# Optimization experiments

Measured on AMD Instinct MI355X. Metric: run time of the kernel, lower is better.

The kernel has to match this reference:

```python
import jax, jax.numpy as jnp
import numpy as np

D_MODEL = 1024
N_HEAD = 16


def setup_inputs() -> dict:
    key = jax.random.key(0)
    ks = jax.random.split(key, 13)
    B, S, D = 2, 2048, D_MODEL
    scale = 1.0 / np.sqrt(D)
    inp = {
        "q": jax.random.normal(ks[0], (B, S, D), jnp.float32),
        "k": jax.random.normal(ks[1], (B, S, D), jnp.float32),
        "v": jax.random.normal(ks[2], (B, S, D), jnp.float32),
        "mask": jax.random.randint(ks[3], (1, 1, S, S), 0, 2, jnp.int32),
        "Wq": jax.random.normal(ks[4], (D, D), jnp.float32) * scale,
        "bq": jnp.zeros((D,), jnp.float32),
        "Wk": jax.random.normal(ks[5], (D, D), jnp.float32) * scale,
        "bk": jnp.zeros((D,), jnp.float32),
        "Wv": jax.random.normal(ks[6], (D, D), jnp.float32) * scale,
        "bv": jnp.zeros((D,), jnp.float32),
        "Wo": jax.random.normal(ks[7], (D, D), jnp.float32) * scale,
        "bo": jnp.zeros((D,), jnp.float32),
    }
    return inp


def _split_heads(x, n_head):
    # [B, S, D] -> [B, H, S, Dh]
    B, S, D = x.shape
    return x.reshape(B, S, n_head, D // n_head).transpose(0, 2, 1, 3)


def reference(q, k, v, mask, Wq, bq, Wk, bk, Wv, bv, Wo, bo):
    # linear projections (torch Linear: x @ W.T + b)
    qp = q @ Wq.T + bq
    kp = k @ Wk.T + bk
    vp = v @ Wv.T + bv
    qh = _split_heads(qp, N_HEAD)  # [B,H,S,Dh]
    kh = _split_heads(kp, N_HEAD)
    vh = _split_heads(vp, N_HEAD)
    d_k = qh.shape[-1]
    scores = jnp.einsum("bhqd,bhkd->bhqk", qh, kh) / jnp.sqrt(jnp.asarray(d_k, qh.dtype))
    neg = jnp.finfo(qh.dtype).min
    scores = jnp.where(mask == 0, neg, scores)
    attn = jax.nn.softmax(scores, axis=-1)
    out = jnp.einsum("bhqk,bhkd->bhqd", attn, vh)  # [B,H,S,Dh]
    B, H, S, Dh = out.shape
    concat = out.transpose(0, 2, 1, 3).reshape(B, S, H * Dh)
    return concat @ Wo.T + bo
```

## Files before the change

### kernel.cpp

```cpp
#include <hip/hip_runtime.h>
#include <hip/hip_bf16.h>

typedef __attribute__((ext_vector_type(8))) short short8;
typedef __attribute__((ext_vector_type(4))) float f32x4;
typedef __attribute__((ext_vector_type(4))) float floatv4;
typedef __attribute__((ext_vector_type(4))) unsigned int u32x4;
typedef unsigned short u16;
typedef unsigned int u32;
typedef unsigned long long u64;

#define S_LEN 2048
#define DMODEL 1024
#define NHEAD 16
#define DHEAD 64

__device__ __forceinline__ u16 f2bf(float f) {
  __hip_bfloat16 h = __float2bfloat16(f);
  return __builtin_bit_cast(u16, h);
}

__device__ __forceinline__ u32 cvtpk(float lo, float hi) {
  u32 r;
  asm("v_cvt_pk_bf16_f32 %0, %1, %2" : "=v"(r) : "v"(lo), "v"(hi));
  return r;
}

__device__ __forceinline__ void gload16(const void* g, void* l) {
  __builtin_amdgcn_global_load_lds(
      (const __attribute__((address_space(1))) u32*)g,
      (__attribute__((address_space(3))) u32*)l, 16, 0, 0);
}

__device__ __forceinline__ f32x4 mfma16(short8 a, short8 b, f32x4 c) {
  return __builtin_amdgcn_mfma_f32_16x16x32_bf16(a, b, c, 0, 0, 0);
}

__global__ void k_convert_qkv(const float* __restrict__ q, const float* __restrict__ k,
                              const float* __restrict__ v, u16* __restrict__ qb,
                              u16* __restrict__ kb, u16* __restrict__ vb) {
  const float* src = blockIdx.y == 0 ? q : blockIdx.y == 1 ? k : v;
  u16* dst = blockIdx.y == 0 ? qb : blockIdx.y == 1 ? kb : vb;
  int i = blockIdx.x * blockDim.x + threadIdx.x;
  floatv4 w = reinterpret_cast<const floatv4*>(src)[i];
  ushort4 o;
  o.x = f2bf(w.x); o.y = f2bf(w.y); o.z = f2bf(w.z); o.w = f2bf(w.w);
  reinterpret_cast<ushort4*>(dst)[i] = o;
}

__global__ void k_convert_w(const float* __restrict__ w0, const float* __restrict__ w1,
                            const float* __restrict__ w2, const float* __restrict__ w3,
                            u16* __restrict__ d0, u16* __restrict__ d1,
                            u16* __restrict__ d2, u16* __restrict__ d3) {
  const int z = blockIdx.y;
  const float* src = z == 0 ? w0 : z == 1 ? w1 : z == 2 ? w2 : w3;
  u16* dst = z == 0 ? d0 : z == 1 ? d1 : z == 2 ? d2 : d3;
  int i = blockIdx.x * blockDim.x + threadIdx.x;
  floatv4 w = reinterpret_cast<const floatv4*>(src)[i];
  ushort4 o;
  o.x = f2bf(w.x); o.y = f2bf(w.y); o.z = f2bf(w.z); o.w = f2bf(w.w);
  reinterpret_cast<ushort4*>(dst)[i] = o;
}

__global__ void k_maskpack(const int* __restrict__ mask, u64* __restrict__ bits) {
  int tid = blockIdx.x * blockDim.x + threadIdx.x;
  u64 b = __ballot(mask[tid] != 0);
  if ((threadIdx.x & 63) == 0) bits[tid >> 6] = b;
}

template <int BN>
__device__ __forceinline__ void gemm_body(const u16* __restrict__ A,
                                          const u16* __restrict__ W,
                                          const float* __restrict__ bias,
                                          void* __restrict__ dst, int mode,
                                          float scale) {
  constexpr int BM = 128, BK = 32, K = DMODEL;
  constexpr int MI = (BN == 128) ? 4 : 2;
  __shared__ u16 As[2][BM * BK];
  __shared__ u16 Bs[2][BN * BK];
  const int t = threadIdx.x;
  const int lane = t & 63, w = t >> 6;
  const int lr = lane & 15, lg = lane >> 4;
  const int wrow = (BN == 128) ? (w >> 1) * 64 : w * 32;
  const int wcol = (BN == 128) ? (w & 1) * 64 : 0;
  const int brow = blockIdx.y * BM, bcol = blockIdx.x * BN;

  const int sr = t >> 2, scg = (t & 3) * 8;
  const u16* Abase = A + (size_t)(brow + sr) * K + scg;
  const u16* Wbase = W + (size_t)(bcol + sr) * K + scg;

  f32x4 acc[MI][4] = {};

  auto stage = [&](int buf, int kt) {
    const int k0 = kt * BK;
    gload16(Abase + k0, &As[buf][w * 512]);
    gload16(Abase + (size_t)64 * K + k0, &As[buf][2048 + w * 512]);
    gload16(Wbase + k0, &Bs[buf][w * 512]);
    if constexpr (BN == 128)
      gload16(Wbase + (size_t)64 * K + k0, &Bs[buf][2048 + w * 512]);
  };

  stage(0, 0);
  __syncthreads();

  int cur = 0;
  constexpr int NT = K / BK;
  for (int kt = 0; kt < NT; ++kt) {
    if (kt + 1 < NT) stage(cur ^ 1, kt + 1);
    short8 af[MI], bfr[4];
#pragma unroll
    for (int i = 0; i < MI; ++i)
      af[i] = *(const short8*)&As[cur][(wrow + i * 16 + lr) * BK + lg * 8];
#pragma unroll
    for (int j = 0; j < 4; ++j)
      bfr[j] = *(const short8*)&Bs[cur][(wcol + j * 16 + lr) * BK + lg * 8];
#pragma unroll
    for (int i = 0; i < MI; ++i)
#pragma unroll
      for (int j = 0; j < 4; ++j)
        acc[i][j] = mfma16(af[i], bfr[j], acc[i][j]);
    __syncthreads();
    cur ^= 1;
  }

#pragma unroll
  for (int i = 0; i < MI; ++i) {
#pragma unroll
    for (int j = 0; j < 4; ++j) {
#pragma unroll
      for (int r = 0; r < 4; ++r) {
        const int m = brow + wrow + i * 16 + lg * 4 + r;
        const int n = bcol + wcol + j * 16 + lr;
        const float v = (acc[i][j][r] + bias[n]) * scale;
        if (mode == 0) {
          const int b = m >> 11, s = m & (S_LEN - 1), h = n >> 6, dh = n & 63;
          ((u16*)dst)[((size_t)(b * NHEAD + h) * S_LEN + s) * DHEAD + dh] = f2bf(v);
        } else if (mode == 1) {
          const int b = m >> 11, s = m & (S_LEN - 1), h = n >> 6, dh = n & 63;
          ((u16*)dst)[((size_t)(b * NHEAD + h) * DHEAD + dh) * S_LEN + s] = f2bf(v);
        } else {
          ((float*)dst)[(size_t)m * DMODEL + n] = v;
        }
      }
    }
  }
}

__global__ __launch_bounds__(256, 2) void k_gemm_qkv(
    const u16* __restrict__ qb, const u16* __restrict__ kb, const u16* __restrict__ vb,
    const u16* __restrict__ Wqb, const u16* __restrict__ Wkb, const u16* __restrict__ Wvb,
    const float* __restrict__ bq, const float* __restrict__ bk, const float* __restrict__ bv,
    u16* __restrict__ qh, u16* __restrict__ kh, u16* __restrict__ vT) {
  const int z = blockIdx.z;
  const u16* A = z == 0 ? qb : z == 1 ? kb : vb;
  const u16* W = z == 0 ? Wqb : z == 1 ? Wkb : Wvb;
  const float* b = z == 0 ? bq : z == 1 ? bk : bv;
  void* dst = z == 0 ? (void*)qh : z == 1 ? (void*)kh : (void*)vT;
  const float scale = z == 0 ? 0.125f * 1.44269504f : 1.0f;
  gemm_body<128>(A, W, b, dst, z == 2 ? 1 : 0, scale);
}

__global__ __launch_bounds__(256, 2) void k_gemm_out(
    const u16* __restrict__ A, const u16* __restrict__ W,
    const float* __restrict__ bias, float* __restrict__ dst) {
  gemm_body<64>(A, W, bias, dst, 2, 1.0f);
}

__global__ __launch_bounds__(256, 4) void k_attn(
    const u16* __restrict__ Qh, const u16* __restrict__ Kh,
    const u16* __restrict__ Vt, const u64* __restrict__ Mb,
    u16* __restrict__ O) {
  constexpr int KB = 64;
  constexpr int NT = S_LEN / KB;
  constexpr int VP = 72;
  __shared__ u16 Ks[2][KB * DHEAD];
  __shared__ u16 Vs[2][DHEAD * VP];
  const int t = threadIdx.x, lane = t & 63, w = t >> 6;
  const int lr = lane & 15, lg = lane >> 4;
  const int qt = blockIdx.x, bh = blockIdx.y;
  const size_t base = (size_t)bh * S_LEN * DHEAD;
  const int q0 = qt * 64;
  const int qrow = q0 + w * 16 + lr;

  short8 qf[2];
  {
    const u16* qp = Qh + base + (size_t)qrow * DHEAD + lg * 8;
    qf[0] = *(const short8*)qp;
    qf[1] = *(const short8*)(qp + 32);
  }

  short8 ones8;
  {
    u32x4 ov = {0x3F803F80u, 0x3F803F80u, 0x3F803F80u, 0x3F803F80u};
    ones8 = __builtin_bit_cast(short8, ov);
  }

  f32x4 oacc[4] = {};
  f32x4 lacc = {};

  const int sr = t >> 3;
  const int scg_k = (((t & 7) ^ (sr & 7)) * 8);
  const int c8 = (t & 7) * 8;

  auto stageK = [&](int buf, int kt2) {
    const int kb0 = kt2 * KB;
    gload16(Kh + base + (size_t)(kb0 + sr) * DHEAD + scg_k, &Ks[buf][w * 512]);
    gload16(Kh + base + (size_t)(kb0 + 32 + sr) * DHEAD + scg_k, &Ks[buf][2048 + w * 512]);
  };
  const u16* vsrc0 = Vt + base + (size_t)sr * S_LEN + c8;
  const u16* vsrc1 = Vt + base + (size_t)(sr + 32) * S_LEN + c8;

  short8 va = *(const short8*)(vsrc0);
  short8 vbr = *(const short8*)(vsrc1);
  stageK(0, 0);
  *(short8*)&Vs[0][sr * VP + c8] = va;
  *(short8*)&Vs[0][(sr + 32) * VP + c8] = vbr;
  __syncthreads();

  u64 mw_next = Mb[(size_t)qrow * (S_LEN / 64)];

  const int rsw = lr & 7;
  const int kc0 = (lg ^ rsw) * 8, kc1 = ((lg + 4) ^ rsw) * 8;

  int cur = 0;
  for (int kt2 = 0; kt2 < NT; ++kt2) {
    const u64 mw = mw_next;
    if (kt2 + 1 < NT) {
      mw_next = Mb[(size_t)qrow * (S_LEN / 64) + kt2 + 1];
      const int kb1 = (kt2 + 1) * KB;
      va = *(const short8*)(vsrc0 + kb1);
      vbr = *(const short8*)(vsrc1 + kb1);
      stageK(cur ^ 1, kt2 + 1);
    }

    f32x4 sc[4];
#pragma unroll
    for (int j = 0; j < 4; ++j) {
      f32x4 c = {};
      short8 k0 = *(const short8*)&Ks[cur][(j * 16 + lr) * 64 + kc0];
      short8 k1 = *(const short8*)&Ks[cur][(j * 16 + lr) * 64 + kc1];
      c = mfma16(k0, qf[0], c);
      c = mfma16(k1, qf[1], c);
      sc[j] = c;
    }

    const u32 mlo = (u32)(mw >> (lg * 4));
    const u32 mhi = (u32)(mw >> (32 + lg * 4));
#pragma unroll
    for (int j = 0; j < 4; ++j) {
      const u32 msrc = (j < 2) ? mlo : mhi;
      const int sh = (j & 1) * 16;
#pragma unroll
      for (int r = 0; r < 4; ++r)
        sc[j][r] = ((msrc >> (sh + r)) & 1u) ? sc[j][r] : -1e30f;
    }

#pragma unroll
    for (int j = 0; j < 4; ++j)
#pragma unroll
      for (int r = 0; r < 4; ++r) sc[j][r] = exp2f(sc[j][r] - 8.0f);

    u32x4 pa1 = {cvtpk(sc[0][0], sc[0][1]), cvtpk(sc[0][2], sc[0][3]),
                 cvtpk(sc[1][0], sc[1][1]), cvtpk(sc[1][2], sc[1][3])};
    u32x4 pa2 = {cvtpk(sc[2][0], sc[2][1]), cvtpk(sc[2][2], sc[2][3]),
                 cvtpk(sc[3][0], sc[3][1]), cvtpk(sc[3][2], sc[3][3])};
    short8 A1 = __builtin_bit_cast(short8, pa1);
    short8 A2 = __builtin_bit_cast(short8, pa2);

    lacc = mfma16(A1, ones8, lacc);
    lacc = mfma16(A2, ones8, lacc);

#pragma unroll
    for (int jo = 0; jo < 4; ++jo) {
      const u16* Vrow = &Vs[cur][(jo * 16 + lr) * VP + lg * 4];
      union { ushort4 h[2]; short8 s8; } vb1, vb2;
      vb1.h[0] = *(const ushort4*)&Vrow[0];
      vb1.h[1] = *(const ushort4*)&Vrow[16];
      vb2.h[0] = *(const ushort4*)&Vrow[32];
      vb2.h[1] = *(const ushort4*)&Vrow[48];
      oacc[jo] = mfma16(A1, vb1.s8, oacc[jo]);
      oacc[jo] = mfma16(A2, vb2.s8, oacc[jo]);
    }

    if (kt2 + 1 < NT) {
      *(short8*)&Vs[cur ^ 1][sr * VP + c8] = va;
      *(short8*)&Vs[cur ^ 1][(sr + 32) * VP + c8] = vbr;
    }
    __syncthreads();
    cur ^= 1;
  }

  const int b = bh >> 4, h = bh & 15;
  float inv[4];
#pragma unroll
  for (int r = 0; r < 4; ++r) inv[r] = 1.0f / fmaxf(lacc[r], 1e-30f);
#pragma unroll
  for (int jo = 0; jo < 4; ++jo)
#pragma unroll
    for (int r = 0; r < 4; ++r) {
      const int s = q0 + w * 16 + lg * 4 + r;
      const float o = oacc[jo][r] * inv[r];
      O[((size_t)(b * S_LEN + s)) * DMODEL + h * DHEAD + jo * 16 + lr] = f2bf(o);
    }
}

extern "C" void kernel_launch(void* const* d_in, const int* in_sizes, int n_in,
                              void* d_out, int out_size, void* d_ws, size_t ws_size,
                              hipStream_t stream) {
  const float* q = (const float*)d_in[0];
  const float* k = (const float*)d_in[1];
  const float* v = (const float*)d_in[2];
  const int* mask = (const int*)d_in[3];
  const float* Wq = (const float*)d_in[4];
  const float* bq = (const float*)d_in[5];
  const float* Wk = (const float*)d_in[6];
  const float* bk = (const float*)d_in[7];
  const float* Wv = (const float*)d_in[8];
  const float* bv = (const float*)d_in[9];
  const float* Wo = (const float*)d_in[10];
  const float* bo = (const float*)d_in[11];

  char* ws = (char*)d_ws;
  const size_t MB = 1024 * 1024;
  u16* qb  = (u16*)(ws + 0 * MB);
  u16* kb  = (u16*)(ws + 8 * MB);
  u16* vb  = (u16*)(ws + 16 * MB);
  u16* Wqb = (u16*)(ws + 24 * MB);
  u16* Wkb = (u16*)(ws + 26 * MB);
  u16* Wvb = (u16*)(ws + 28 * MB);
  u16* Wob = (u16*)(ws + 30 * MB);
  u16* qh  = (u16*)(ws + 32 * MB);
  u16* kh  = (u16*)(ws + 40 * MB);
  u16* vT  = (u16*)(ws + 48 * MB);
  u16* cc  = (u16*)(ws + 56 * MB);
  u64* mb  = (u64*)(ws + 64 * MB);

  k_convert_qkv<<<dim3(4096, 3), 256, 0, stream>>>(q, k, v, qb, kb, vb);
  k_convert_w<<<dim3(1024, 4), 256, 0, stream>>>(Wq, Wk, Wv, Wo, Wqb, Wkb, Wvb, Wob);
  k_maskpack<<<16384, 256, 0, stream>>>(mask, mb);

  k_gemm_qkv<<<dim3(8, 32, 3), 256, 0, stream>>>(qb, kb, vb, Wqb, Wkb, Wvb,
                                                 bq, bk, bv, qh, kh, vT);

  k_attn<<<dim3(S_LEN / 64, 32), 256, 0, stream>>>(qh, kh, vT, mb, cc);

  k_gemm_out<<<dim3(16, 32), 256, 0, stream>>>(cc, Wob, bo, (float*)d_out);
}
```

Before: 166.7 us.

## Process two query row-tiles per wave in attention to reuse K/V fragments

Each attention block now covers 128 query rows instead of 64, with every wave computing two 16-row tiles (A and B) that share the same K and V fragments loaded from shared memory. This halves the K/V global staging and LDS reads per query row and raises MFMA work per LDS load. In exchange, register pressure doubles for accumulators, occupancy bounds drop to 2 blocks per CU, and the grid shrinks to 512 blocks.

```diff
diff --git a/kernel.cpp b/kernel.cpp
--- a/kernel.cpp
+++ b/kernel.cpp
@@ -165,7 +165,7 @@
   gemm_body<64>(A, W, bias, dst, 2, 1.0f);
 }
 
-__global__ __launch_bounds__(256, 4) void k_attn(
+__global__ __launch_bounds__(256, 2) void k_attn(
     const u16* __restrict__ Qh, const u16* __restrict__ Kh,
     const u16* __restrict__ Vt, const u64* __restrict__ Mb,
     u16* __restrict__ O) {
@@ -178,14 +178,18 @@
   const int lr = lane & 15, lg = lane >> 4;
   const int qt = blockIdx.x, bh = blockIdx.y;
   const size_t base = (size_t)bh * S_LEN * DHEAD;
-  const int q0 = qt * 64;
-  const int qrow = q0 + w * 16 + lr;
-
-  short8 qf[2];
+  const int q0 = qt * 128;
+  const int qrowA = q0 + w * 32 + lr;
+  const int qrowB = qrowA + 16;
+
+  short8 qfA[2], qfB[2];
   {
-    const u16* qp = Qh + base + (size_t)qrow * DHEAD + lg * 8;
-    qf[0] = *(const short8*)qp;
-    qf[1] = *(const short8*)(qp + 32);
+    const u16* qpA = Qh + base + (size_t)qrowA * DHEAD + lg * 8;
+    qfA[0] = *(const short8*)qpA;
+    qfA[1] = *(const short8*)(qpA + 32);
+    const u16* qpB = Qh + base + (size_t)qrowB * DHEAD + lg * 8;
+    qfB[0] = *(const short8*)qpB;
+    qfB[1] = *(const short8*)(qpB + 32);
   }
 
   short8 ones8;
@@ -194,8 +198,8 @@
     ones8 = __builtin_bit_cast(short8, ov);
   }
 
-  f32x4 oacc[4] = {};
-  f32x4 lacc = {};
+  f32x4 oaccA[4] = {}, oaccB[4] = {};
+  f32x4 laccA = {}, laccB = {};
 
   const int sr = t >> 3;
   const int scg_k = (((t & 7) ^ (sr & 7)) * 8);
@@ -216,58 +220,84 @@
   *(short8*)&Vs[0][(sr + 32) * VP + c8] = vbr;
   __syncthreads();
 
-  u64 mw_next = Mb[(size_t)qrow * (S_LEN / 64)];
+  u64 mwA_next = Mb[(size_t)qrowA * (S_LEN / 64)];
+  u64 mwB_next = Mb[(size_t)qrowB * (S_LEN / 64)];
 
   const int rsw = lr & 7;
   const int kc0 = (lg ^ rsw) * 8, kc1 = ((lg + 4) ^ rsw) * 8;
 
   int cur = 0;
   for (int kt2 = 0; kt2 < NT; ++kt2) {
-    const u64 mw = mw_next;
+    const u64 mwA = mwA_next, mwB = mwB_next;
     if (kt2 + 1 < NT) {
-      mw_next = Mb[(size_t)qrow * (S_LEN / 64) + kt2 + 1];
+      mwA_next = Mb[(size_t)qrowA * (S_LEN / 64) + kt2 + 1];
+      mwB_next = Mb[(size_t)qrowB * (S_LEN / 64) + kt2 + 1];
       const int kb1 = (kt2 + 1) * KB;
       va = *(const short8*)(vsrc0 + kb1);
       vbr = *(const short8*)(vsrc1 + kb1);
       stageK(cur ^ 1, kt2 + 1);
     }
 
-    f32x4 sc[4];
+    f32x4 scA[4], scB[4];
 #pragma unroll
     for (int j = 0; j < 4; ++j) {
-      f32x4 c = {};
       short8 k0 = *(const short8*)&Ks[cur][(j * 16 + lr) * 64 + kc0];
       short8 k1 = *(const short8*)&Ks[cur][(j * 16 + lr) * 64 + kc1];
-      c = mfma16(k0, qf[0], c);
-      c = mfma16(k1, qf[1], c);
-      sc[j] = c;
-    }
-
-    const u32 mlo = (u32)(mw >> (lg * 4));
-    const u32 mhi = (u32)(mw >> (32 + lg * 4));
-#pragma unroll
-    for (int j = 0; j < 4; ++j) {
-      const u32 msrc = (j < 2) ? mlo : mhi;
-      const int sh = (j & 1) * 16;
-#pragma unroll
-      for (int r = 0; r < 4; ++r)
-        sc[j][r] = ((msrc >> (sh + r)) & 1u) ? sc[j][r] : -1e30f;
-    }
-
-#pragma unroll
-    for (int j = 0; j < 4; ++j)
-#pragma unroll
-      for (int r = 0; r < 4; ++r) sc[j][r] = exp2f(sc[j][r] - 8.0f);
-
-    u32x4 pa1 = {cvtpk(sc[0][0], sc[0][1]), cvtpk(sc[0][2], sc[0][3]),
-                 cvtpk(sc[1][0], sc[1][1]), cvtpk(sc[1][2], sc[1][3])};
-    u32x4 pa2 = {cvtpk(sc[2][0], sc[2][1]), cvtpk(sc[2][2], sc[2][3]),
-                 cvtpk(sc[3][0], sc[3][1]), cvtpk(sc[3][2], sc[3][3])};
-    short8 A1 = __builtin_bit_cast(short8, pa1);
-    short8 A2 = __builtin_bit_cast(short8, pa2);
-
-    lacc = mfma16(A1, ones8, lacc);
-    lacc = mfma16(A2, ones8, lacc);
+      f32x4 cA = {}, cB = {};
+      cA = mfma16(k0, qfA[0], cA);
+      cA = mfma16(k1, qfA[1], cA);
+      cB = mfma16(k0, qfB[0], cB);
+      cB = mfma16(k1, qfB[1], cB);
+      scA[j] = cA;
+      scB[j] = cB;
+    }
+
+    {
+      const u32 mlo = (u32)(mwA >> (lg * 4));
+      const u32 mhi = (u32)(mwA >> (32 + lg * 4));
+#pragma unroll
+      for (int j = 0; j < 4; ++j) {
+        const u32 msrc = (j < 2) ? mlo : mhi;
+        const int sh = (j & 1) * 16;
+#pragma unroll
+        for (int r = 0; r < 4; ++r) {
+          float s = ((msrc >> (sh + r)) & 1u) ? scA[j][r] : -1e30f;
+          scA[j][r] = exp2f(s - 8.0f);
+        }
+      }
+    }
+    {
+      const u32 mlo = (u32)(mwB >> (lg * 4));
+      const u32 mhi = (u32)(mwB >> (32 + lg * 4));
+#pragma unroll
+      for (int j = 0; j < 4; ++j) {
+        const u32 msrc = (j < 2) ? mlo : mhi;
+        const int sh = (j & 1) * 16;
+#pragma unroll
+        for (int r = 0; r < 4; ++r) {
+          float s = ((msrc >> (sh + r)) & 1u) ? scB[j][r] : -1e30f;
+          scB[j][r] = exp2f(s - 8.0f);
+        }
+      }
+    }
+
+    u32x4 pa1A = {cvtpk(scA[0][0], scA[0][1]), cvtpk(scA[0][2], scA[0][3]),
+                  cvtpk(scA[1][0], scA[1][1]), cvtpk(scA[1][2], scA[1][3])};
+    u32x4 pa2A = {cvtpk(scA[2][0], scA[2][1]), cvtpk(scA[2][2], scA[2][3]),
+                  cvtpk(scA[3][0], scA[3][1]), cvtpk(scA[3][2], scA[3][3])};
+    u32x4 pa1B = {cvtpk(scB[0][0], scB[0][1]), cvtpk(scB[0][2], scB[0][3]),
+                  cvtpk(scB[1][0], scB[1][1]), cvtpk(scB[1][2], scB[1][3])};
+    u32x4 pa2B = {cvtpk(scB[2][0], scB[2][1]), cvtpk(scB[2][2], scB[2][3]),
+                  cvtpk(scB[3][0], scB[3][1]), cvtpk(scB[3][2], scB[3][3])};
+    short8 A1a = __builtin_bit_cast(short8, pa1A);
+    short8 A2a = __builtin_bit_cast(short8, pa2A);
+    short8 A1b = __builtin_bit_cast(short8, pa1B);
+    short8 A2b = __builtin_bit_cast(short8, pa2B);
+
+    laccA = mfma16(A1a, ones8, laccA);
+    laccA = mfma16(A2a, ones8, laccA);
+    laccB = mfma16(A1b, ones8, laccB);
+    laccB = mfma16(A2b, ones8, laccB);
 
 #pragma unroll
     for (int jo = 0; jo < 4; ++jo) {
@@ -277,8 +307,10 @@
       vb1.h[1] = *(const ushort4*)&Vrow[16];
       vb2.h[0] = *(const ushort4*)&Vrow[32];
       vb2.h[1] = *(const ushort4*)&Vrow[48];
-      oacc[jo] = mfma16(A1, vb1.s8, oacc[jo]);
-      oacc[jo] = mfma16(A2, vb2.s8, oacc[jo]);
+      oaccA[jo] = mfma16(A1a, vb1.s8, oaccA[jo]);
+      oaccA[jo] = mfma16(A2a, vb2.s8, oaccA[jo]);
+      oaccB[jo] = mfma16(A1b, vb1.s8, oaccB[jo]);
+      oaccB[jo] = mfma16(A2b, vb2.s8, oaccB[jo]);
     }
 
     if (kt2 + 1 < NT) {
@@ -290,16 +322,22 @@
   }
 
   const int b = bh >> 4, h = bh & 15;
-  float inv[4];
-#pragma unroll
-  for (int r = 0; r < 4; ++r) inv[r] = 1.0f / fmaxf(lacc[r], 1e-30f);
+  float invA[4], invB[4];
+#pragma unroll
+  for (int r = 0; r < 4; ++r) {
+    invA[r] = 1.0f / fmaxf(laccA[r], 1e-30f);
+    invB[r] = 1.0f / fmaxf(laccB[r], 1e-30f);
+  }
 #pragma unroll
   for (int jo = 0; jo < 4; ++jo)
 #pragma unroll
     for (int r = 0; r < 4; ++r) {
-      const int s = q0 + w * 16 + lg * 4 + r;
-      const float o = oacc[jo][r] * inv[r];
-      O[((size_t)(b * S_LEN + s)) * DMODEL + h * DHEAD + jo * 16 + lr] = f2bf(o);
+      const int sA = q0 + w * 32 + lg * 4 + r;
+      const float oA = oaccA[jo][r] * invA[r];
+      O[((size_t)(b * S_LEN + sA)) * DMODEL + h * DHEAD + jo * 16 + lr] = f2bf(oA);
+      const int sB = sA + 16;
+      const float oB = oaccB[jo][r] * invB[r];
+      O[((size_t)(b * S_LEN + sB)) * DMODEL + h * DHEAD + jo * 16 + lr] = f2bf(oB);
     }
 }
 
@@ -341,7 +379,7 @@
   k_gemm_qkv<<<dim3(8, 32, 3), 256, 0, stream>>>(qb, kb, vb, Wqb, Wkb, Wvb,
                                                  bq, bk, bv, qh, kh, vT);
 
-  k_attn<<<dim3(S_LEN / 64, 32), 256, 0, stream>>>(qh, kh, vT, mb, cc);
+  k_attn<<<dim3(S_LEN / 128, 32), 256, 0, stream>>>(qh, kh, vT, mb, cc);
 
   k_gemm_out<<<dim3(16, 32), 256, 0, stream>>>(cc, Wob, bo, (float*)d_out);
 }
```

After: 171.9 us. 3.1% more time.

## Merge prep kernels into one launch and remap attention block order

Applied to the files above, without the earlier changes.

Folds the qkv conversion, weight conversion and mask packing kernels into a single launch that branches on block index, removing two kernel launches and their inter-kernel gaps. It also remaps the attention grid so blocks running concurrently cover 8 heads per query tile group, which changes which K/V data stays in L2 across neighbouring blocks. The mapping is a bijection over the 1024 blocks, so the work done is unchanged, but cache locality may shift.

```diff
diff --git a/kernel.cpp b/kernel.cpp
--- a/kernel.cpp
+++ b/kernel.cpp
@@ -35,36 +35,39 @@
   return __builtin_amdgcn_mfma_f32_16x16x32_bf16(a, b, c, 0, 0, 0);
 }
 
-__global__ void k_convert_qkv(const float* __restrict__ q, const float* __restrict__ k,
-                              const float* __restrict__ v, u16* __restrict__ qb,
-                              u16* __restrict__ kb, u16* __restrict__ vb) {
-  const float* src = blockIdx.y == 0 ? q : blockIdx.y == 1 ? k : v;
-  u16* dst = blockIdx.y == 0 ? qb : blockIdx.y == 1 ? kb : vb;
-  int i = blockIdx.x * blockDim.x + threadIdx.x;
-  floatv4 w = reinterpret_cast<const floatv4*>(src)[i];
-  ushort4 o;
-  o.x = f2bf(w.x); o.y = f2bf(w.y); o.z = f2bf(w.z); o.w = f2bf(w.w);
-  reinterpret_cast<ushort4*>(dst)[i] = o;
-}
-
-__global__ void k_convert_w(const float* __restrict__ w0, const float* __restrict__ w1,
-                            const float* __restrict__ w2, const float* __restrict__ w3,
-                            u16* __restrict__ d0, u16* __restrict__ d1,
-                            u16* __restrict__ d2, u16* __restrict__ d3) {
-  const int z = blockIdx.y;
-  const float* src = z == 0 ? w0 : z == 1 ? w1 : z == 2 ? w2 : w3;
-  u16* dst = z == 0 ? d0 : z == 1 ? d1 : z == 2 ? d2 : d3;
-  int i = blockIdx.x * blockDim.x + threadIdx.x;
-  floatv4 w = reinterpret_cast<const floatv4*>(src)[i];
-  ushort4 o;
-  o.x = f2bf(w.x); o.y = f2bf(w.y); o.z = f2bf(w.z); o.w = f2bf(w.w);
-  reinterpret_cast<ushort4*>(dst)[i] = o;
-}
-
-__global__ void k_maskpack(const int* __restrict__ mask, u64* __restrict__ bits) {
-  int tid = blockIdx.x * blockDim.x + threadIdx.x;
-  u64 b = __ballot(mask[tid] != 0);
-  if ((threadIdx.x & 63) == 0) bits[tid >> 6] = b;
+__global__ void k_prep(const float* __restrict__ q, const float* __restrict__ k,
+                       const float* __restrict__ v,
+                       const float* __restrict__ Wq, const float* __restrict__ Wk,
+                       const float* __restrict__ Wv, const float* __restrict__ Wo,
+                       const int* __restrict__ mask,
+                       u16* __restrict__ qb, u16* __restrict__ kb, u16* __restrict__ vb,
+                       u16* __restrict__ Wqb, u16* __restrict__ Wkb,
+                       u16* __restrict__ Wvb, u16* __restrict__ Wob,
+                       u64* __restrict__ bits) {
+  const int bid = blockIdx.x;
+  if (bid < 12288) {
+    const int z = bid >> 12;
+    const int i = (bid & 4095) * 256 + threadIdx.x;
+    const float* src = z == 0 ? q : z == 1 ? k : v;
+    u16* dst = z == 0 ? qb : z == 1 ? kb : vb;
+    floatv4 w = reinterpret_cast<const floatv4*>(src)[i];
+    ushort4 o;
+    o.x = f2bf(w.x); o.y = f2bf(w.y); o.z = f2bf(w.z); o.w = f2bf(w.w);
+    reinterpret_cast<ushort4*>(dst)[i] = o;
+  } else if (bid < 16384) {
+    const int z = (bid - 12288) >> 10;
+    const int i = ((bid - 12288) & 1023) * 256 + threadIdx.x;
+    const float* src = z == 0 ? Wq : z == 1 ? Wk : z == 2 ? Wv : Wo;
+    u16* dst = z == 0 ? Wqb : z == 1 ? Wkb : z == 2 ? Wvb : Wob;
+    floatv4 w = reinterpret_cast<const floatv4*>(src)[i];
+    ushort4 o;
+    o.x = f2bf(w.x); o.y = f2bf(w.y); o.z = f2bf(w.z); o.w = f2bf(w.w);
+    reinterpret_cast<ushort4*>(dst)[i] = o;
+  } else {
+    const int tid = (bid - 16384) * 256 + threadIdx.x;
+    u64 b = __ballot(mask[tid] != 0);
+    if ((threadIdx.x & 63) == 0) bits[tid >> 6] = b;
+  }
 }
 
 template <int BN>
@@ -176,7 +179,9 @@
   __shared__ u16 Vs[2][DHEAD * VP];
   const int t = threadIdx.x, lane = t & 63, w = t >> 6;
   const int lr = lane & 15, lg = lane >> 4;
-  const int qt = blockIdx.x, bh = blockIdx.y;
+  const int lid = blockIdx.y * 32 + blockIdx.x;
+  const int qt = (lid >> 3) & 31;
+  const int bh = (lid & 7) + ((lid >> 8) << 3);
   const size_t base = (size_t)bh * S_LEN * DHEAD;
   const int q0 = qt * 64;
   const int qrow = q0 + w * 16 + lr;
@@ -334,9 +339,8 @@
   u16* cc  = (u16*)(ws + 56 * MB);
   u64* mb  = (u64*)(ws + 64 * MB);
 
-  k_convert_qkv<<<dim3(4096, 3), 256, 0, stream>>>(q, k, v, qb, kb, vb);
-  k_convert_w<<<dim3(1024, 4), 256, 0, stream>>>(Wq, Wk, Wv, Wo, Wqb, Wkb, Wvb, Wob);
-  k_maskpack<<<16384, 256, 0, stream>>>(mask, mb);
+  k_prep<<<32768, 256, 0, stream>>>(q, k, v, Wq, Wk, Wv, Wo, mask,
+                                    qb, kb, vb, Wqb, Wkb, Wvb, Wob, mb);
 
   k_gemm_qkv<<<dim3(8, 32, 3), 256, 0, stream>>>(qb, kb, vb, Wqb, Wkb, Wvb,
                                                  bq, bk, bv, qh, kh, vT);
```

Measured after the change: 161.8 us. 1.03x faster.
